# Optimization experiments

Hardware: AMD Instinct MI355X
Metric: run time of the kernel (lower is better)

Reference implementation:

```python
import jax, jax.numpy as jnp
import numpy as np

LN_EPS = 1e-5
L2_EPS = 1e-12
SCALE = 8.0

def setup_inputs() -> dict:
    key = jax.random.key(0)
    k0, k1, k2 = jax.random.split(key, 3)
    b, c, H, W = 16, 256, 64, 64
    heads, dim_head = 8, 32
    dim_inner = heads * dim_head  # 256
    x = jax.random.normal(k0, (b, c, H, W), dtype=jnp.float32)
    ln_gamma = jnp.ones((c,), jnp.float32)
    ln_beta = jnp.zeros((c,), jnp.float32)
    W_qkv = jax.random.normal(k1, (c, 3 * dim_inner), dtype=jnp.float32) * 0.02
    temperature = jnp.ones((heads,), jnp.float32)
    W_out = jax.random.normal(k2, (dim_inner, c), dtype=jnp.float32) * 0.02
    b_out = jnp.zeros((c,), jnp.float32)
    return {"x": x, "ln_gamma": ln_gamma, "ln_beta": ln_beta, "W_qkv": W_qkv,
            "temperature": temperature, "W_out": W_out, "b_out": b_out, "heads": heads}

def _l2norm(t):
    # F.normalize(t, dim=-1): divide by clamped L2 norm along last axis
    n = jnp.sqrt(jnp.sum(t * t, axis=-1, keepdims=True))
    return t / jnp.maximum(n, L2_EPS)

def reference(x, ln_gamma, ln_beta, W_qkv, temperature, W_out, b_out, heads):
    b, c, H, W = x.shape
    n = H * W
    dim_head = W_qkv.shape[1] // (3 * heads)
    # b c h w -> b (h w) c
    t = jnp.transpose(x, (0, 2, 3, 1)).reshape(b, n, c)
    # LayerNorm over channel dim (affine)
    mu = jnp.mean(t, axis=-1, keepdims=True)
    var = jnp.mean(jnp.square(t - mu), axis=-1, keepdims=True)
    t = (t - mu) * jax.lax.rsqrt(var + LN_EPS) * ln_gamma + ln_beta
    # qkv projection; split last dim as (qkv, heads, dim_head) -> (3, b, h, d, n)
    qkv = (t @ W_qkv).reshape(b, n, 3, heads, dim_head)
    qkv = jnp.transpose(qkv, (2, 0, 3, 4, 1))
    q, k, v = qkv[0], qkv[1], qkv[2]
    q = _l2norm(q) * jnp.exp(temperature)[None, :, None, None]
    k = _l2norm(k)
    # cross-covariance attention over channel dim: sim is [b, h, d, d]
    sim = jnp.einsum('bhin,bhjn->bhij', q, k) * SCALE
    attn = jax.nn.softmax(sim, axis=-1)
    out = jnp.einsum('bhij,bhjn->bhin', attn, v)  # [b, h, d, n]
    # b h d n -> b n (h d)
    out = jnp.transpose(out, (0, 3, 1, 2)).reshape(b, n, heads * dim_head)
    out = out @ W_out + b_out
    # b (h w) c -> b c h w
    return jnp.transpose(out.reshape(b, H, W, c), (0, 3, 1, 2))
```

## Files before the change

### kernel.cpp

```cpp
#include <hip/hip_runtime.h>

typedef unsigned short u16;
typedef __bf16 bf16x8 __attribute__((ext_vector_type(8)));
typedef float f32x4 __attribute__((ext_vector_type(4)));

#define MFMA(a, b, c) __builtin_amdgcn_mfma_f32_16x16x32_bf16((a), (b), (c), 0, 0, 0)

__device__ __forceinline__ u16 f2bf(float f) {
    unsigned u = __float_as_uint(f);
    unsigned r = (u + 0x7fffu + ((u >> 16) & 1u)) >> 16;
    return (u16)r;
}
__device__ __forceinline__ float bf2f(u16 h) { return __uint_as_float(((unsigned)h) << 16); }

typedef unsigned int u32_g __attribute__((address_space(1)));
typedef unsigned int u32_l __attribute__((address_space(3)));
__device__ __forceinline__ void gload16(const void* g, void* l) {
    __builtin_amdgcn_global_load_lds((const u32_g*)g, (u32_l*)l, 16, 0, 0);
}


__global__ __launch_bounds__(256) void k_ln(const float* __restrict__ x,
                                            const float* __restrict__ gamma,
                                            const float* __restrict__ beta,
                                            u16* __restrict__ xlnT) {
    int bid = blockIdx.x;
    int b = bid >> 6, nt = bid & 63;
    int nb = nt * 64;
    __shared__ unsigned xsu[256 * 33];
    __shared__ float muv[64], rsv[64];
    __shared__ float redS[8 * 64], redS2[8 * 64];
    int t = threadIdx.x;
    {
        int np = t & 31;
        int c0 = t >> 5;
        const float* xp = x + ((size_t)b * 256) * 4096 + nb + np * 2;
        for (int i = 0; i < 32; i++) {
            int c = c0 + i * 8;
            float2 f = *(const float2*)(xp + (size_t)c * 4096);
            unsigned u = (unsigned)f2bf(f.x) | ((unsigned)f2bf(f.y) << 16);
            xsu[c * 33 + np] = u;
        }
    }
    __syncthreads();
    {
        int np = t & 31, q = t >> 5;
        float s0 = 0, s20 = 0, s1 = 0, s21 = 0;
        for (int i = 0; i < 32; i++) {
            unsigned u = xsu[(q * 32 + i) * 33 + np];
            float a = bf2f((u16)(u & 0xffffu));
            float bv = bf2f((u16)(u >> 16));
            s0 += a; s20 += a * a; s1 += bv; s21 += bv * bv;
        }
        redS[q * 64 + np * 2] = s0;  redS[q * 64 + np * 2 + 1] = s1;
        redS2[q * 64 + np * 2] = s20; redS2[q * 64 + np * 2 + 1] = s21;
    }
    __syncthreads();
    if (t < 64) {
        float s = 0, s2 = 0;
        for (int q = 0; q < 8; q++) { s += redS[q * 64 + t]; s2 += redS2[q * 64 + t]; }
        float m = s * (1.f / 256.f);
        float var = s2 * (1.f / 256.f) - m * m;
        muv[t] = m;
        rsv[t] = rsqrtf(var + 1e-5f);
    }
    __syncthreads();
    {
        int c4 = (t & 63) * 4;
        int ng = t >> 6;
        float g[4], e[4];
        for (int j = 0; j < 4; j++) { g[j] = gamma[c4 + j]; e[j] = beta[c4 + j]; }
        for (int i = 0; i < 16; i++) {
            int n = ng * 16 + i;
            float m = muv[n], rs = rsv[n];
            u16 h[4];
            for (int j = 0; j < 4; j++) {
                unsigned u = xsu[(c4 + j) * 33 + (n >> 1)];
                u16 raw = (n & 1) ? (u16)(u >> 16) : (u16)(u & 0xffffu);
                float v = (bf2f(raw) - m) * rs * g[j] + e[j];
                h[j] = f2bf(v);
            }
            uint2 w2;
            w2.x = (unsigned)h[0] | ((unsigned)h[1] << 16);
            w2.y = (unsigned)h[2] | ((unsigned)h[3] << 16);
            *(uint2*)(xlnT + ((size_t)(b * 4096 + nb + n)) * 256 + c4) = w2;
        }
    }
}

__global__ __launch_bounds__(256) void k_prep(const float* __restrict__ Wqkv,
                                              const float* __restrict__ Wout,
                                              u16* __restrict__ WqkvT, u16* __restrict__ WoutT,
                                              float* __restrict__ sims, float* __restrict__ normsq) {
    int i = blockIdx.x * 256 + threadIdx.x;
    if (i < 768 * 256) { int o = i >> 8, c = i & 255; WqkvT[i] = f2bf(Wqkv[c * 768 + o]); }
    if (i < 256 * 256) { int o = i >> 8, c = i & 255; WoutT[i] = f2bf(Wout[c * 256 + o]); }
    if (i < 128 * 1024) sims[i] = 0.f;
    if (i < 16 * 512) normsq[i] = 0.f;
}

__global__ __launch_bounds__(256) void k_gemm(const u16* __restrict__ A, size_t aStrB,
                                              const u16* __restrict__ Bb, size_t bStrB,
                                              int mtiles, int mrow0,
                                              u16* __restrict__ o16,
                                              float* __restrict__ o32, const float* __restrict__ bias,
                                              int mode) {
    extern __shared__ __align__(16) u16 smem[];
    u16* aT = smem;
    u16* bT = smem + 128 * 32;
    int bid = blockIdx.x;
    int per_b = mtiles * 32;
    int b = bid / per_b;
    int r2 = bid % per_b;
    int mbase = mrow0 + (r2 >> 5) * 128, nbase = (r2 & 31) * 128;
    int t = threadIdx.x, w = t >> 6, lane = t & 63, l15 = lane & 15, quad = lane >> 4;
    const u16* Ap = A + (size_t)b * aStrB;
    const u16* Bp = Bb + (size_t)b * bStrB;
    int srow = lane >> 2;
    int g8 = (((lane & 3) ^ ((lane >> 3) & 3)) << 3);
    const u16* gA = Ap + (size_t)(mbase + w * 32 + srow) * 256 + g8;
    const u16* gB = Bp + (size_t)(nbase + w * 32 + srow) * 256 + g8;
    u16* lA = aT + w * 1024;
    u16* lB = bT + w * 1024;
    int cOff = ((quad ^ ((l15 >> 1) & 3)) << 3);
    f32x4 acc[2][8];
    f32x4 z = {0.f, 0.f, 0.f, 0.f};
    for (int fm = 0; fm < 2; fm++)
        for (int fn = 0; fn < 8; fn++) acc[fm][fn] = z;
    for (int kt = 0; kt < 8; kt++) {
        int kb = kt * 32;
        if (kt) __syncthreads();
        gload16(gA + kb, lA);
        gload16(gA + 16 * 256 + kb, lA + 512);
        gload16(gB + kb, lB);
        gload16(gB + 16 * 256 + kb, lB + 512);
        __syncthreads();
        bf16x8 af0 = *(const bf16x8*)&aT[(w * 32 + l15) * 32 + cOff];
        bf16x8 af1 = *(const bf16x8*)&aT[(w * 32 + 16 + l15) * 32 + cOff];
        for (int fn = 0; fn < 8; fn++) {
            bf16x8 bfr = *(const bf16x8*)&bT[(fn * 16 + l15) * 32 + cOff];
            acc[0][fn] = MFMA(af0, bfr, acc[0][fn]);
            acc[1][fn] = MFMA(af1, bfr, acc[1][fn]);
        }
    }
    if (mode == 0) {
        for (int fm = 0; fm < 2; fm++)
            for (int fn = 0; fn < 8; fn++)
                for (int r = 0; r < 4; r++) {
                    int row = mbase + w * 32 + fm * 16 + quad * 4 + r;
                    int col = nbase + fn * 16 + l15;
                    o16[((size_t)b * 512 + row) * 4096 + col] = f2bf(acc[fm][fn][r]);
                }
    } else if (mode == 1) {
        for (int fm = 0; fm < 2; fm++)
            for (int fn = 0; fn < 8; fn++)
                for (int r = 0; r < 4; r++) {
                    int row = mbase + w * 32 + fm * 16 + quad * 4 + r;
                    int col = nbase + fn * 16 + l15;
                    o32[((size_t)b * 256 + row) * 4096 + col] = acc[fm][fn][r] + bias[row];
                }
    } else {
        __syncthreads();
        u16* tp = smem;
        for (int fm = 0; fm < 2; fm++)
            for (int fn = 0; fn < 8; fn++) {
                unsigned p01 = (unsigned)f2bf(acc[fm][fn][0]) | ((unsigned)f2bf(acc[fm][fn][1]) << 16);
                unsigned p23 = (unsigned)f2bf(acc[fm][fn][2]) | ((unsigned)f2bf(acc[fm][fn][3]) << 16);
                uint2 pk; pk.x = p01; pk.y = p23;
                *(uint2*)&tp[(fn * 16 + l15) * 136 + w * 32 + fm * 16 + quad * 4] = pk;
            }
        __syncthreads();
        int jb0 = mbase - 512;
        for (int p = 0; p < 8; p++) {
            int col = p * 16 + (t >> 4);
            int ch = t & 15;
            uint4 v = *(const uint4*)&tp[col * 136 + ch * 8];
            *(uint4*)(o16 + ((size_t)b * 4096 + nbase + col) * 256 + jb0 + ch * 8) = v;
        }
    }
}

__global__ __launch_bounds__(256) void k_sim(const u16* __restrict__ qk, float* __restrict__ sims,
                                             float* __restrict__ normsq) {
    int bid = blockIdx.x;
    int ns = bid & 7, bh = bid >> 3;
    int b = bh >> 3, h = bh & 7;
    __shared__ u16 qs[32 * 264];
    __shared__ u16 ks[32 * 264];
    int t = threadIdx.x, w = t >> 6, lane = t & 63, l15 = lane & 15, quad = lane >> 4;
    int ib = w >> 1, jb = w & 1;
    const u16* qbase = qk + ((size_t)(b * 512) + h * 32) * 4096;
    const u16* kbase = qk + ((size_t)(b * 512) + 256 + h * 32) * 4096;
    int col8 = t & 31, rb = t >> 5;
    f32x4 acc = {0.f, 0.f, 0.f, 0.f};
    float sq[4] = {0.f, 0.f, 0.f, 0.f}, sk[4] = {0.f, 0.f, 0.f, 0.f};
    for (int kc = 0; kc < 2; kc++) {
        int kb = ns * 512 + kc * 256;
        if (kc) __syncthreads();
#pragma unroll
        for (int i = 0; i < 4; i++) {
            int r = rb + i * 8;
            uint4 pq = *(const uint4*)(qbase + (size_t)r * 4096 + kb + col8 * 8);
            *(uint4*)&qs[r * 264 + col8 * 8] = pq;
            const u16* us = (const u16*)&pq;
#pragma unroll
            for (int jj = 0; jj < 8; jj++) { float f = bf2f(us[jj]); sq[i] += f * f; }
            uint4 pk = *(const uint4*)(kbase + (size_t)r * 4096 + kb + col8 * 8);
            *(uint4*)&ks[r * 264 + col8 * 8] = pk;
            const u16* uk = (const u16*)&pk;
#pragma unroll
            for (int jj = 0; jj < 8; jj++) { float f = bf2f(uk[jj]); sk[i] += f * f; }
        }
        __syncthreads();
        for (int s = 0; s < 8; s++) {
            bf16x8 a = *(const bf16x8*)&qs[(ib * 16 + l15) * 264 + s * 32 + quad * 8];
            bf16x8 bb = *(const bf16x8*)&ks[(jb * 16 + l15) * 264 + s * 32 + quad * 8];
            acc = MFMA(a, bb, acc);
        }
    }
#pragma unroll
    for (int i = 0; i < 4; i++) {
#pragma unroll
        for (int m = 16; m >= 1; m >>= 1) {
            sq[i] += __shfl_xor(sq[i], m, 32);
            sk[i] += __shfl_xor(sk[i], m, 32);
        }
    }
    if (col8 == 0) {
#pragma unroll
        for (int i = 0; i < 4; i++) {
            atomicAdd(normsq + b * 512 + h * 32 + rb + i * 8, sq[i]);
            atomicAdd(normsq + b * 512 + 256 + h * 32 + rb + i * 8, sk[i]);
        }
    }
    float* sp = sims + (size_t)bh * 1024;
    for (int r = 0; r < 4; r++) {
        int row = ib * 16 + quad * 4 + r, col = jb * 16 + l15;
        atomicAdd(sp + row * 32 + col, acc[r]);
    }
}

__global__ __launch_bounds__(256) void k_softmw(const float* __restrict__ sims,
                                                const float* __restrict__ normsq,
                                                const float* __restrict__ temp,
                                                const u16* __restrict__ WoutT,
                                                u16* __restrict__ Mb) {
    int bh = blockIdx.x;
    int b = bh >> 3, h = bh & 7;
    __shared__ float as[32 * 32];
    __shared__ float scq[32], sck[32];
    int t = threadIdx.x;
    if (t < 32)
        scq[t] = expf(temp[h]) * 8.0f / fmaxf(sqrtf(normsq[b * 512 + h * 32 + t]), 1e-12f);
    else if (t < 64) {
        int d = t - 32;
        sck[d] = 1.0f / fmaxf(sqrtf(normsq[b * 512 + 256 + h * 32 + d]), 1e-12f);
    }
    __syncthreads();
    if (t < 32) {
        float row[32];
        float m = -1e30f;
        const float* sp = sims + (size_t)bh * 1024 + t * 32;
        float sq = scq[t];
#pragma unroll
        for (int j = 0; j < 32; j++) { float v = sp[j] * sq * sck[j]; row[j] = v; m = fmaxf(m, v); }
        float s = 0.f;
#pragma unroll
        for (int j = 0; j < 32; j++) { float p = expf(row[j] - m); row[j] = p; s += p; }
        float inv = 1.f / s;
#pragma unroll
        for (int j = 0; j < 32; j++) as[t * 32 + j] = row[j] * inv;
    }
    __syncthreads();
    float wv[32];
    const u16* wp = WoutT + (size_t)t * 256 + h * 32;
#pragma unroll
    for (int d = 0; d < 32; d++) wv[d] = bf2f(wp[d]);
    u16* mp = Mb + ((size_t)b * 256 + t) * 256 + h * 32;
    for (int j0 = 0; j0 < 32; j0 += 8) {
        u16 hh[8];
#pragma unroll
        for (int jj = 0; jj < 8; jj++) {
            int j = j0 + jj;
            float s = 0.f;
#pragma unroll
            for (int d = 0; d < 32; d++) s += wv[d] * as[d * 32 + j];
            hh[jj] = f2bf(s);
        }
        uint4 pk;
        pk.x = (unsigned)hh[0] | ((unsigned)hh[1] << 16);
        pk.y = (unsigned)hh[2] | ((unsigned)hh[3] << 16);
        pk.z = (unsigned)hh[4] | ((unsigned)hh[5] << 16);
        pk.w = (unsigned)hh[6] | ((unsigned)hh[7] << 16);
        *(uint4*)(mp + j0) = pk;
    }
}

extern "C" void kernel_launch(void* const* d_in, const int* in_sizes, int n_in,
                              void* d_out, int out_size, void* d_ws, size_t ws_size,
                              hipStream_t stream) {
    const float* x     = (const float*)d_in[0];
    const float* gamma = (const float*)d_in[1];
    const float* beta  = (const float*)d_in[2];
    const float* Wqkv  = (const float*)d_in[3];
    const float* temp  = (const float*)d_in[4];
    const float* Wout  = (const float*)d_in[5];
    const float* bout  = (const float*)d_in[6];
    float* out = (float*)d_out;

    char* ws = (char*)d_ws;
    size_t off = 0;
    auto alloc = [&](size_t nbytes) -> void* {
        void* p = ws + off;
        off = (off + nbytes + 255) & ~(size_t)255;
        return p;
    };
    u16* xlnT    = (u16*)alloc((size_t)16 * 4096 * 256 * 2);
    u16* WqkvT   = (u16*)alloc((size_t)768 * 256 * 2);
    u16* WoutT   = (u16*)alloc((size_t)256 * 256 * 2);
    u16* qk      = (u16*)alloc((size_t)16 * 512 * 4096 * 2);
    u16* vT      = (u16*)alloc((size_t)16 * 4096 * 256 * 2);
    u16* Mb      = (u16*)alloc((size_t)16 * 256 * 256 * 2);
    float* normsq = (float*)alloc((size_t)16 * 512 * 4);
    float* sims   = (float*)alloc((size_t)128 * 1024 * 4);
    (void)ws_size; (void)in_sizes; (void)n_in; (void)out_size;

    hipLaunchKernelGGL(k_ln, dim3(1024), dim3(256), 0, stream, x, gamma, beta, xlnT);
    hipLaunchKernelGGL(k_prep, dim3(768), dim3(256), 0, stream, Wqkv, Wout, WqkvT, WoutT, sims, normsq);
    hipLaunchKernelGGL(k_gemm, dim3(2048), dim3(256), 16384, stream,
                       WqkvT, (size_t)0, xlnT, (size_t)4096 * 256, 4, 0,
                       qk, (float*)nullptr, (const float*)nullptr, 0);
    hipLaunchKernelGGL(k_gemm, dim3(1024), dim3(256), 34816, stream,
                       WqkvT, (size_t)0, xlnT, (size_t)4096 * 256, 2, 512,
                       vT, (float*)nullptr, (const float*)nullptr, 2);
    hipLaunchKernelGGL(k_sim, dim3(1024), dim3(256), 0, stream, qk, sims, normsq);
    hipLaunchKernelGGL(k_softmw, dim3(128), dim3(256), 0, stream, sims, normsq, temp, WoutT, Mb);
    hipLaunchKernelGGL(k_gemm, dim3(1024), dim3(256), 16384, stream,
                       Mb, (size_t)256 * 256, vT, (size_t)4096 * 256, 2, 0,
                       (u16*)nullptr, out, bout, 1);
}
```

Before: 231.9 us.

## Compute channel attention via Gram matrix of normalized input instead of materializing QKV

Rather than projecting the full sequence to q/k/v, the new code builds the per-batch channel Gram matrix G = X·Xᵀ of the layer-normed input. It then derives q·kᵀ similarities and the q/k norms as Wq·G·Wkᵀ and diag(Wq·G·Wqᵀ), using hi/lo bf16 splits to keep precision. The attention matrix is folded with W_out and W_v into a single 256x256 matrix per batch, applied with one GEMM on the normed input. This removes the large qk and v intermediates and their GEMMs, but adds an extra channel-major LN output, a split-K partial Gram buffer with a reduction kernel, and several small low-parallelism kernels (128 or 64 blocks).

```diff
diff --git a/kernel.cpp b/kernel.cpp
--- a/kernel.cpp
+++ b/kernel.cpp
@@ -23,7 +23,7 @@
 __global__ __launch_bounds__(256) void k_ln(const float* __restrict__ x,
                                             const float* __restrict__ gamma,
                                             const float* __restrict__ beta,
-                                            u16* __restrict__ xlnT) {
+                                            u16* __restrict__ xlnT, u16* __restrict__ xcn) {
     int bid = blockIdx.x;
     int b = bid >> 6, nt = bid & 63;
     int nb = nt * 64;
@@ -86,33 +86,171 @@
             *(uint2*)(xlnT + ((size_t)(b * 4096 + nb + n)) * 256 + c4) = w2;
         }
     }
+    {
+        int lr = t & 7;
+        int n0 = lr * 8;
+        for (int it = 0; it < 8; it++) {
+            int cg = (t >> 3) + it * 32;
+            float g = gamma[cg], e = beta[cg];
+            u16 hh[8];
+            for (int jj = 0; jj < 8; jj++) {
+                int nn = n0 + jj;
+                unsigned u = xsu[cg * 33 + (nn >> 1)];
+                u16 raw = (nn & 1) ? (u16)(u >> 16) : (u16)(u & 0xffffu);
+                float v = (bf2f(raw) - muv[nn]) * rsv[nn] * g + e;
+                hh[jj] = f2bf(v);
+            }
+            uint4 pk;
+            pk.x = (unsigned)hh[0] | ((unsigned)hh[1] << 16);
+            pk.y = (unsigned)hh[2] | ((unsigned)hh[3] << 16);
+            pk.z = (unsigned)hh[4] | ((unsigned)hh[5] << 16);
+            pk.w = (unsigned)hh[6] | ((unsigned)hh[7] << 16);
+            *(uint4*)(xcn + ((size_t)(b * 256 + cg)) * 4096 + nb + n0) = pk;
+        }
+    }
 }
 
 __global__ __launch_bounds__(256) void k_prep(const float* __restrict__ Wqkv,
                                               const float* __restrict__ Wout,
-                                              u16* __restrict__ WqkvT, u16* __restrict__ WoutT,
-                                              float* __restrict__ sims, float* __restrict__ normsq) {
+                                              u16* __restrict__ WqkvT, u16* __restrict__ WvTn,
+                                              u16* __restrict__ WoutT) {
     int i = blockIdx.x * 256 + threadIdx.x;
-    if (i < 768 * 256) { int o = i >> 8, c = i & 255; WqkvT[i] = f2bf(Wqkv[c * 768 + o]); }
-    if (i < 256 * 256) { int o = i >> 8, c = i & 255; WoutT[i] = f2bf(Wout[c * 256 + o]); }
-    if (i < 128 * 1024) sims[i] = 0.f;
-    if (i < 16 * 512) normsq[i] = 0.f;
+    if (i < 512 * 256) { int o = i >> 8, c = i & 255; WqkvT[i] = f2bf(Wqkv[c * 768 + o]); }
+    if (i < 256 * 256) {
+        int e = i >> 8, o = i & 255;
+        WvTn[i] = f2bf(Wqkv[e * 768 + 512 + o]);
+        WoutT[i] = f2bf(Wout[o * 256 + e]);
+    }
+}
+
+__global__ __launch_bounds__(256) void k_gram(const u16* __restrict__ xcn, float* __restrict__ Gp) {
+    int bid = blockIdx.x;
+    int s = bid & 7, tile = (bid >> 3) & 3, b = bid >> 5;
+    int tm = tile >> 1, tn = tile & 1;
+    __shared__ __align__(16) u16 aT[128 * 32];
+    __shared__ __align__(16) u16 bT[128 * 32];
+    int t = threadIdx.x, w = t >> 6, lane = t & 63, l15 = lane & 15, quad = lane >> 4;
+    int srow = lane >> 2;
+    int g8 = (((lane & 3) ^ ((lane >> 3) & 3)) << 3);
+    const u16* xb = xcn + (size_t)b * 256 * 4096 + (size_t)s * 512;
+    const u16* gA = xb + (size_t)(tm * 128 + w * 32 + srow) * 4096 + g8;
+    const u16* gB = xb + (size_t)(tn * 128 + w * 32 + srow) * 4096 + g8;
+    u16* lA = aT + w * 1024;
+    u16* lB = bT + w * 1024;
+    int cOff = ((quad ^ ((l15 >> 1) & 3)) << 3);
+    f32x4 acc[2][8];
+    f32x4 z = {0.f, 0.f, 0.f, 0.f};
+    for (int fm = 0; fm < 2; fm++)
+        for (int fn = 0; fn < 8; fn++) acc[fm][fn] = z;
+    for (int kt = 0; kt < 16; kt++) {
+        int kb = kt * 32;
+        if (kt) __syncthreads();
+        gload16(gA + kb, lA);
+        gload16(gA + 16 * 4096 + kb, lA + 512);
+        gload16(gB + kb, lB);
+        gload16(gB + 16 * 4096 + kb, lB + 512);
+        __syncthreads();
+        bf16x8 af0 = *(const bf16x8*)&aT[(w * 32 + l15) * 32 + cOff];
+        bf16x8 af1 = *(const bf16x8*)&aT[(w * 32 + 16 + l15) * 32 + cOff];
+        for (int fn = 0; fn < 8; fn++) {
+            bf16x8 bfr = *(const bf16x8*)&bT[(fn * 16 + l15) * 32 + cOff];
+            acc[0][fn] = MFMA(af0, bfr, acc[0][fn]);
+            acc[1][fn] = MFMA(af1, bfr, acc[1][fn]);
+        }
+    }
+    float* gp = Gp + (size_t)(s * 16 + b) * 65536;
+    for (int fm = 0; fm < 2; fm++)
+        for (int fn = 0; fn < 8; fn++)
+            for (int r = 0; r < 4; r++) {
+                int row = tm * 128 + w * 32 + fm * 16 + quad * 4 + r;
+                int col = tn * 128 + fn * 16 + l15;
+                gp[row * 256 + col] = acc[fm][fn][r];
+            }
+}
+
+__global__ __launch_bounds__(256) void k_g2b(const float* __restrict__ Gp,
+                                             u16* __restrict__ Ghi, u16* __restrict__ Glo) {
+    int idx = blockIdx.x * 256 + threadIdx.x;
+    const float4* p = (const float4*)Gp + idx;
+    float4 s = p[0];
+#pragma unroll
+    for (int j = 1; j < 8; j++) {
+        float4 v = p[(size_t)j * 262144];
+        s.x += v.x; s.y += v.y; s.z += v.z; s.w += v.w;
+    }
+    u16 h0 = f2bf(s.x), h1 = f2bf(s.y), h2 = f2bf(s.z), h3 = f2bf(s.w);
+    u16 l0 = f2bf(s.x - bf2f(h0)), l1 = f2bf(s.y - bf2f(h1));
+    u16 l2 = f2bf(s.z - bf2f(h2)), l3 = f2bf(s.w - bf2f(h3));
+    uint2 ph; ph.x = (unsigned)h0 | ((unsigned)h1 << 16); ph.y = (unsigned)h2 | ((unsigned)h3 << 16);
+    uint2 pl; pl.x = (unsigned)l0 | ((unsigned)l1 << 16); pl.y = (unsigned)l2 | ((unsigned)l3 << 16);
+    *(uint2*)(Ghi + (size_t)idx * 4) = ph;
+    *(uint2*)(Glo + (size_t)idx * 4) = pl;
+}
+
+__global__ __launch_bounds__(256) void k_sq(const u16* __restrict__ A,
+                                            const u16* __restrict__ Ghi, const u16* __restrict__ Glo,
+                                            u16* __restrict__ Shi, u16* __restrict__ Slo) {
+    __shared__ __align__(16) u16 aT[128 * 32];
+    __shared__ __align__(16) u16 bT[128 * 32];
+    int bid = blockIdx.x;
+    int b = bid >> 3;
+    int r2 = bid & 7;
+    int mbase = (r2 >> 1) * 128, nbase = (r2 & 1) * 128;
+    int t = threadIdx.x, w = t >> 6, lane = t & 63, l15 = lane & 15, quad = lane >> 4;
+    int srow = lane >> 2;
+    int g8 = (((lane & 3) ^ ((lane >> 3) & 3)) << 3);
+    const u16* gA = A + (size_t)(mbase + w * 32 + srow) * 256 + g8;
+    const u16* gBh = Ghi + (size_t)b * 65536 + (size_t)(nbase + w * 32 + srow) * 256 + g8;
+    const u16* gBl = Glo + (size_t)b * 65536 + (size_t)(nbase + w * 32 + srow) * 256 + g8;
+    u16* lA = aT + w * 1024;
+    u16* lB = bT + w * 1024;
+    int cOff = ((quad ^ ((l15 >> 1) & 3)) << 3);
+    f32x4 acc[2][8];
+    f32x4 z = {0.f, 0.f, 0.f, 0.f};
+    for (int fm = 0; fm < 2; fm++)
+        for (int fn = 0; fn < 8; fn++) acc[fm][fn] = z;
+    for (int kt = 0; kt < 16; kt++) {
+        int kb = (kt & 7) * 32;
+        const u16* gB = (kt < 8) ? gBh : gBl;
+        if (kt) __syncthreads();
+        gload16(gA + kb, lA);
+        gload16(gA + 16 * 256 + kb, lA + 512);
+        gload16(gB + kb, lB);
+        gload16(gB + 16 * 256 + kb, lB + 512);
+        __syncthreads();
+        bf16x8 af0 = *(const bf16x8*)&aT[(w * 32 + l15) * 32 + cOff];
+        bf16x8 af1 = *(const bf16x8*)&aT[(w * 32 + 16 + l15) * 32 + cOff];
+        for (int fn = 0; fn < 8; fn++) {
+            bf16x8 bfr = *(const bf16x8*)&bT[(fn * 16 + l15) * 32 + cOff];
+            acc[0][fn] = MFMA(af0, bfr, acc[0][fn]);
+            acc[1][fn] = MFMA(af1, bfr, acc[1][fn]);
+        }
+    }
+    for (int fm = 0; fm < 2; fm++)
+        for (int fn = 0; fn < 8; fn++)
+            for (int r = 0; r < 4; r++) {
+                int row = mbase + w * 32 + fm * 16 + quad * 4 + r;
+                int col = nbase + fn * 16 + l15;
+                float v = acc[fm][fn][r];
+                u16 hi = f2bf(v);
+                Shi[((size_t)b * 512 + row) * 256 + col] = hi;
+                Slo[((size_t)b * 512 + row) * 256 + col] = f2bf(v - bf2f(hi));
+            }
 }
 
 __global__ __launch_bounds__(256) void k_gemm(const u16* __restrict__ A, size_t aStrB,
                                               const u16* __restrict__ Bb, size_t bStrB,
-                                              int mtiles, int mrow0,
-                                              u16* __restrict__ o16,
-                                              float* __restrict__ o32, const float* __restrict__ bias,
-                                              int mode) {
-    extern __shared__ __align__(16) u16 smem[];
-    u16* aT = smem;
-    u16* bT = smem + 128 * 32;
+                                              int mtiles, int ntiles,
+                                              u16* __restrict__ o16, float* __restrict__ o32,
+                                              const float* __restrict__ bias,
+                                              size_t oStrB, int oRstr, int mode) {
+    __shared__ __align__(16) u16 aT[128 * 32];
+    __shared__ __align__(16) u16 bT[128 * 32];
     int bid = blockIdx.x;
-    int per_b = mtiles * 32;
+    int per_b = mtiles * ntiles;
     int b = bid / per_b;
     int r2 = bid % per_b;
-    int mbase = mrow0 + (r2 >> 5) * 128, nbase = (r2 & 31) * 128;
+    int mbase = (r2 / ntiles) * 128, nbase = (r2 % ntiles) * 128;
     int t = threadIdx.x, w = t >> 6, lane = t & 63, l15 = lane & 15, quad = lane >> 4;
     const u16* Ap = A + (size_t)b * aStrB;
     const u16* Bp = Bb + (size_t)b * bStrB;
@@ -149,150 +287,126 @@
                 for (int r = 0; r < 4; r++) {
                     int row = mbase + w * 32 + fm * 16 + quad * 4 + r;
                     int col = nbase + fn * 16 + l15;
-                    o16[((size_t)b * 512 + row) * 4096 + col] = f2bf(acc[fm][fn][r]);
+                    o16[(size_t)b * oStrB + (size_t)row * oRstr + col] = f2bf(acc[fm][fn][r]);
                 }
-    } else if (mode == 1) {
+    } else {
         for (int fm = 0; fm < 2; fm++)
             for (int fn = 0; fn < 8; fn++)
                 for (int r = 0; r < 4; r++) {
                     int row = mbase + w * 32 + fm * 16 + quad * 4 + r;
                     int col = nbase + fn * 16 + l15;
-                    o32[((size_t)b * 256 + row) * 4096 + col] = acc[fm][fn][r] + bias[row];
+                    o32[(size_t)b * oStrB + (size_t)row * oRstr + col] = acc[fm][fn][r] + bias[row];
                 }
-    } else {
-        __syncthreads();
-        u16* tp = smem;
-        for (int fm = 0; fm < 2; fm++)
-            for (int fn = 0; fn < 8; fn++) {
-                unsigned p01 = (unsigned)f2bf(acc[fm][fn][0]) | ((unsigned)f2bf(acc[fm][fn][1]) << 16);
-                unsigned p23 = (unsigned)f2bf(acc[fm][fn][2]) | ((unsigned)f2bf(acc[fm][fn][3]) << 16);
-                uint2 pk; pk.x = p01; pk.y = p23;
-                *(uint2*)&tp[(fn * 16 + l15) * 136 + w * 32 + fm * 16 + quad * 4] = pk;
-            }
-        __syncthreads();
-        int jb0 = mbase - 512;
-        for (int p = 0; p < 8; p++) {
-            int col = p * 16 + (t >> 4);
-            int ch = t & 15;
-            uint4 v = *(const uint4*)&tp[col * 136 + ch * 8];
-            *(uint4*)(o16 + ((size_t)b * 4096 + nbase + col) * 256 + jb0 + ch * 8) = v;
-        }
-    }
-}
-
-__global__ __launch_bounds__(256) void k_sim(const u16* __restrict__ qk, float* __restrict__ sims,
-                                             float* __restrict__ normsq) {
-    int bid = blockIdx.x;
-    int ns = bid & 7, bh = bid >> 3;
-    int b = bh >> 3, h = bh & 7;
-    __shared__ u16 qs[32 * 264];
-    __shared__ u16 ks[32 * 264];
-    int t = threadIdx.x, w = t >> 6, lane = t & 63, l15 = lane & 15, quad = lane >> 4;
-    int ib = w >> 1, jb = w & 1;
-    const u16* qbase = qk + ((size_t)(b * 512) + h * 32) * 4096;
-    const u16* kbase = qk + ((size_t)(b * 512) + 256 + h * 32) * 4096;
-    int col8 = t & 31, rb = t >> 5;
-    f32x4 acc = {0.f, 0.f, 0.f, 0.f};
-    float sq[4] = {0.f, 0.f, 0.f, 0.f}, sk[4] = {0.f, 0.f, 0.f, 0.f};
-    for (int kc = 0; kc < 2; kc++) {
-        int kb = ns * 512 + kc * 256;
-        if (kc) __syncthreads();
-#pragma unroll
-        for (int i = 0; i < 4; i++) {
-            int r = rb + i * 8;
-            uint4 pq = *(const uint4*)(qbase + (size_t)r * 4096 + kb + col8 * 8);
-            *(uint4*)&qs[r * 264 + col8 * 8] = pq;
-            const u16* us = (const u16*)&pq;
-#pragma unroll
-            for (int jj = 0; jj < 8; jj++) { float f = bf2f(us[jj]); sq[i] += f * f; }
-            uint4 pk = *(const uint4*)(kbase + (size_t)r * 4096 + kb + col8 * 8);
-            *(uint4*)&ks[r * 264 + col8 * 8] = pk;
-            const u16* uk = (const u16*)&pk;
-#pragma unroll
-            for (int jj = 0; jj < 8; jj++) { float f = bf2f(uk[jj]); sk[i] += f * f; }
-        }
-        __syncthreads();
-        for (int s = 0; s < 8; s++) {
-            bf16x8 a = *(const bf16x8*)&qs[(ib * 16 + l15) * 264 + s * 32 + quad * 8];
-            bf16x8 bb = *(const bf16x8*)&ks[(jb * 16 + l15) * 264 + s * 32 + quad * 8];
-            acc = MFMA(a, bb, acc);
-        }
-    }
-#pragma unroll
-    for (int i = 0; i < 4; i++) {
-#pragma unroll
-        for (int m = 16; m >= 1; m >>= 1) {
-            sq[i] += __shfl_xor(sq[i], m, 32);
-            sk[i] += __shfl_xor(sk[i], m, 32);
-        }
-    }
-    if (col8 == 0) {
-#pragma unroll
-        for (int i = 0; i < 4; i++) {
-            atomicAdd(normsq + b * 512 + h * 32 + rb + i * 8, sq[i]);
-            atomicAdd(normsq + b * 512 + 256 + h * 32 + rb + i * 8, sk[i]);
-        }
-    }
-    float* sp = sims + (size_t)bh * 1024;
-    for (int r = 0; r < 4; r++) {
-        int row = ib * 16 + quad * 4 + r, col = jb * 16 + l15;
-        atomicAdd(sp + row * 32 + col, acc[r]);
-    }
-}
-
-__global__ __launch_bounds__(256) void k_softmw(const float* __restrict__ sims,
-                                                const float* __restrict__ normsq,
-                                                const float* __restrict__ temp,
-                                                const u16* __restrict__ WoutT,
-                                                u16* __restrict__ Mb) {
+    }
+}
+
+__global__ __launch_bounds__(256) void k_attn(const u16* __restrict__ Shi,
+                                              const u16* __restrict__ Slo,
+                                              const u16* __restrict__ WqkvT,
+                                              const u16* __restrict__ WoutT,
+                                              const float* __restrict__ temp,
+                                              u16* __restrict__ M_all) {
     int bh = blockIdx.x;
     int b = bh >> 3, h = bh & 7;
-    __shared__ float as[32 * 32];
+    __shared__ u16 sqh[32 * 264], sql[32 * 264], skh[32 * 264], wq[32 * 264], wk[32 * 264];
+    __shared__ u16 wo[256 * 40];
+    __shared__ u16 attnT[32 * 40];
+    __shared__ float simS[32 * 33];
+    __shared__ float redn[4 * 64];
     __shared__ float scq[32], sck[32];
-    int t = threadIdx.x;
+    int t = threadIdx.x, w = t >> 6, lane = t & 63, l15 = lane & 15, quad = lane >> 4;
+    {
+        int r = t >> 3, cc0 = (t & 7) * 32;
+        const u16* gqh = Shi + ((size_t)(b * 512) + h * 32 + r) * 256 + cc0;
+        const u16* gql = Slo + ((size_t)(b * 512) + h * 32 + r) * 256 + cc0;
+        const u16* gkh = Shi + ((size_t)(b * 512) + 256 + h * 32 + r) * 256 + cc0;
+        const u16* gwq = WqkvT + (size_t)(h * 32 + r) * 256 + cc0;
+        const u16* gwk = WqkvT + (size_t)(256 + h * 32 + r) * 256 + cc0;
+#pragma unroll
+        for (int k = 0; k < 4; k++) {
+            *(uint4*)&sqh[r * 264 + cc0 + k * 8] = *(const uint4*)(gqh + k * 8);
+            *(uint4*)&sql[r * 264 + cc0 + k * 8] = *(const uint4*)(gql + k * 8);
+            *(uint4*)&skh[r * 264 + cc0 + k * 8] = *(const uint4*)(gkh + k * 8);
+            *(uint4*)&wq[r * 264 + cc0 + k * 8] = *(const uint4*)(gwq + k * 8);
+            *(uint4*)&wk[r * 264 + cc0 + k * 8] = *(const uint4*)(gwk + k * 8);
+        }
+        const u16* gwo = WoutT + (size_t)t * 256 + h * 32;
+#pragma unroll
+        for (int k = 0; k < 4; k++) *(uint4*)&wo[t * 40 + k * 8] = *(const uint4*)(gwo + k * 8);
+    }
+    __syncthreads();
+    {
+        int rn = t & 63, cc = t >> 6;
+        int e0 = cc * 64;
+        float s = 0.f;
+        if (rn < 32) {
+            const u16* ph = &sqh[rn * 264];
+            const u16* pl = &sql[rn * 264];
+            const u16* pb = &wq[rn * 264];
+            for (int e = 0; e < 64; e++)
+                s += (bf2f(ph[e0 + e]) + bf2f(pl[e0 + e])) * bf2f(pb[e0 + e]);
+        } else {
+            const u16* ph = &skh[(rn - 32) * 264];
+            const u16* pb = &wk[(rn - 32) * 264];
+            for (int e = 0; e < 64; e++)
+                s += bf2f(ph[e0 + e]) * bf2f(pb[e0 + e]);
+        }
+        redn[cc * 64 + rn] = s;
+    }
+    {
+        int iq = w >> 1, jq = w & 1;
+        f32x4 acc = {0.f, 0.f, 0.f, 0.f};
+        for (int s8 = 0; s8 < 8; s8++) {
+            bf16x8 a = *(const bf16x8*)&sqh[(iq * 16 + l15) * 264 + s8 * 32 + quad * 8];
+            bf16x8 bb = *(const bf16x8*)&wk[(jq * 16 + l15) * 264 + s8 * 32 + quad * 8];
+            acc = MFMA(a, bb, acc);
+        }
+        for (int s8 = 0; s8 < 8; s8++) {
+            bf16x8 a = *(const bf16x8*)&sql[(iq * 16 + l15) * 264 + s8 * 32 + quad * 8];
+            bf16x8 bb = *(const bf16x8*)&wk[(jq * 16 + l15) * 264 + s8 * 32 + quad * 8];
+            acc = MFMA(a, bb, acc);
+        }
+        for (int r = 0; r < 4; r++)
+            simS[(iq * 16 + quad * 4 + r) * 33 + jq * 16 + l15] = acc[r];
+    }
+    __syncthreads();
     if (t < 32)
-        scq[t] = expf(temp[h]) * 8.0f / fmaxf(sqrtf(normsq[b * 512 + h * 32 + t]), 1e-12f);
+        scq[t] = expf(temp[h]) * 8.0f /
+                 fmaxf(sqrtf(redn[t] + redn[64 + t] + redn[128 + t] + redn[192 + t]), 1e-12f);
     else if (t < 64) {
         int d = t - 32;
-        sck[d] = 1.0f / fmaxf(sqrtf(normsq[b * 512 + 256 + h * 32 + d]), 1e-12f);
+        sck[d] = 1.0f / fmaxf(sqrtf(redn[32 + d] + redn[96 + d] + redn[160 + d] + redn[224 + d]), 1e-12f);
     }
     __syncthreads();
     if (t < 32) {
         float row[32];
-        float m = -1e30f;
-        const float* sp = sims + (size_t)bh * 1024 + t * 32;
-        float sq = scq[t];
-#pragma unroll
-        for (int j = 0; j < 32; j++) { float v = sp[j] * sq * sck[j]; row[j] = v; m = fmaxf(m, v); }
+        float m = -1e30f, sqv = scq[t];
+#pragma unroll
+        for (int j = 0; j < 32; j++) {
+            float v = simS[t * 33 + j] * sqv * sck[j];
+            row[j] = v; m = fmaxf(m, v);
+        }
         float s = 0.f;
 #pragma unroll
         for (int j = 0; j < 32; j++) { float p = expf(row[j] - m); row[j] = p; s += p; }
         float inv = 1.f / s;
 #pragma unroll
-        for (int j = 0; j < 32; j++) as[t * 32 + j] = row[j] * inv;
-    }
-    __syncthreads();
-    float wv[32];
-    const u16* wp = WoutT + (size_t)t * 256 + h * 32;
-#pragma unroll
-    for (int d = 0; d < 32; d++) wv[d] = bf2f(wp[d]);
-    u16* mp = Mb + ((size_t)b * 256 + t) * 256 + h * 32;
-    for (int j0 = 0; j0 < 32; j0 += 8) {
-        u16 hh[8];
-#pragma unroll
-        for (int jj = 0; jj < 8; jj++) {
-            int j = j0 + jj;
-            float s = 0.f;
-#pragma unroll
-            for (int d = 0; d < 32; d++) s += wv[d] * as[d * 32 + j];
-            hh[jj] = f2bf(s);
-        }
-        uint4 pk;
-        pk.x = (unsigned)hh[0] | ((unsigned)hh[1] << 16);
-        pk.y = (unsigned)hh[2] | ((unsigned)hh[3] << 16);
-        pk.z = (unsigned)hh[4] | ((unsigned)hh[5] << 16);
-        pk.w = (unsigned)hh[6] | ((unsigned)hh[7] << 16);
-        *(uint4*)(mp + j0) = pk;
+        for (int j = 0; j < 32; j++) attnT[j * 40 + t] = f2bf(row[j] * inv);
+    }
+    __syncthreads();
+    {
+        f32x4 z = {0.f, 0.f, 0.f, 0.f};
+        for (int mf = 0; mf < 4; mf++) {
+            bf16x8 a = *(const bf16x8*)&wo[((w * 4 + mf) * 16 + l15) * 40 + quad * 8];
+            for (int nf = 0; nf < 2; nf++) {
+                bf16x8 bb = *(const bf16x8*)&attnT[(nf * 16 + l15) * 40 + quad * 8];
+                f32x4 d = MFMA(a, bb, z);
+                for (int r = 0; r < 4; r++) {
+                    int c = (w * 4 + mf) * 16 + quad * 4 + r;
+                    M_all[((size_t)(b * 256) + c) * 256 + h * 32 + nf * 16 + l15] = f2bf(d[r]);
+                }
+            }
+        }
     }
 }
 
@@ -315,27 +429,32 @@
         off = (off + nbytes + 255) & ~(size_t)255;
         return p;
     };
-    u16* xlnT    = (u16*)alloc((size_t)16 * 4096 * 256 * 2);
-    u16* WqkvT   = (u16*)alloc((size_t)768 * 256 * 2);
-    u16* WoutT   = (u16*)alloc((size_t)256 * 256 * 2);
-    u16* qk      = (u16*)alloc((size_t)16 * 512 * 4096 * 2);
-    u16* vT      = (u16*)alloc((size_t)16 * 4096 * 256 * 2);
-    u16* Mb      = (u16*)alloc((size_t)16 * 256 * 256 * 2);
-    float* normsq = (float*)alloc((size_t)16 * 512 * 4);
-    float* sims   = (float*)alloc((size_t)128 * 1024 * 4);
+    u16* xlnT   = (u16*)alloc((size_t)16 * 4096 * 256 * 2);
+    u16* xcn    = (u16*)alloc((size_t)16 * 256 * 4096 * 2);
+    u16* WqkvT  = (u16*)alloc((size_t)512 * 256 * 2);
+    u16* WvTn   = (u16*)alloc((size_t)256 * 256 * 2);
+    u16* WoutT  = (u16*)alloc((size_t)256 * 256 * 2);
+    float* Gp   = (float*)alloc((size_t)8 * 16 * 65536 * 4);
+    u16* Gbh    = (u16*)alloc((size_t)16 * 65536 * 2);
+    u16* Gbl    = (u16*)alloc((size_t)16 * 65536 * 2);
+    u16* Sqh    = (u16*)alloc((size_t)16 * 512 * 256 * 2);
+    u16* Sql    = (u16*)alloc((size_t)16 * 512 * 256 * 2);
+    u16* M_all  = (u16*)alloc((size_t)16 * 256 * 256 * 2);
+    u16* F      = (u16*)alloc((size_t)16 * 256 * 256 * 2);
     (void)ws_size; (void)in_sizes; (void)n_in; (void)out_size;
 
-    hipLaunchKernelGGL(k_ln, dim3(1024), dim3(256), 0, stream, x, gamma, beta, xlnT);
-    hipLaunchKernelGGL(k_prep, dim3(768), dim3(256), 0, stream, Wqkv, Wout, WqkvT, WoutT, sims, normsq);
-    hipLaunchKernelGGL(k_gemm, dim3(2048), dim3(256), 16384, stream,
-                       WqkvT, (size_t)0, xlnT, (size_t)4096 * 256, 4, 0,
-                       qk, (float*)nullptr, (const float*)nullptr, 0);
-    hipLaunchKernelGGL(k_gemm, dim3(1024), dim3(256), 34816, stream,
-                       WqkvT, (size_t)0, xlnT, (size_t)4096 * 256, 2, 512,
-                       vT, (float*)nullptr, (const float*)nullptr, 2);
-    hipLaunchKernelGGL(k_sim, dim3(1024), dim3(256), 0, stream, qk, sims, normsq);
-    hipLaunchKernelGGL(k_softmw, dim3(128), dim3(256), 0, stream, sims, normsq, temp, WoutT, Mb);
-    hipLaunchKernelGGL(k_gemm, dim3(1024), dim3(256), 16384, stream,
-                       Mb, (size_t)256 * 256, vT, (size_t)4096 * 256, 2, 0,
-                       (u16*)nullptr, out, bout, 1);
-}
+    hipLaunchKernelGGL(k_ln, dim3(1024), dim3(256), 0, stream, x, gamma, beta, xlnT, xcn);
+    hipLaunchKernelGGL(k_prep, dim3(768), dim3(256), 0, stream, Wqkv, Wout, WqkvT, WvTn, WoutT);
+    hipLaunchKernelGGL(k_gram, dim3(512), dim3(256), 0, stream, xcn, Gp);
+    hipLaunchKernelGGL(k_g2b, dim3(1024), dim3(256), 0, stream, Gp, Gbh, Gbl);
+    hipLaunchKernelGGL(k_sq, dim3(128), dim3(256), 0, stream, WqkvT, Gbh, Gbl, Sqh, Sql);
+    hipLaunchKernelGGL(k_attn, dim3(128), dim3(256), 0, stream, Sqh, Sql, WqkvT, WoutT, temp, M_all);
+    hipLaunchKernelGGL(k_gemm, dim3(64), dim3(256), 0, stream,
+                       M_all, (size_t)65536, WvTn, (size_t)0, 2, 2,
+                       F, (float*)nullptr, (const float*)nullptr,
+                       (size_t)65536, 256, 0);
+    hipLaunchKernelGGL(k_gemm, dim3(1024), dim3(256), 0, stream,
+                       F, (size_t)65536, xlnT, (size_t)4096 * 256, 2, 32,
+                       (u16*)nullptr, out, bout,
+                       (size_t)256 * 4096, 4096, 1);
+}
```

New measurement: 218.7 us. -5.7%, faster.
